# Optimization experiments

Hardware: AMD Instinct MI355X
Metric: run time of the kernel (lower is better)

The kernel has to match this reference:

```python
import jax, jax.numpy as jnp
import numpy as np

B = 131072
NF, E = 9, 8
D0 = NF * E  # 72
H = 64       # expert hidden
O = 8        # expert output
T, SE, SH = 3, 3, 3
VOCAB = 160000

PARAM_SHAPES = {
    "emb_table": (VOCAB, E),
    "spec0_W1": (T, SE, D0, H), "spec0_b1": (T, SE, H),
    "spec0_W2": (T, SE, H, O),  "spec0_b2": (T, SE, O),
    "shar0_W1": (SH, D0, H),    "shar0_b1": (SH, H),
    "shar0_W2": (SH, H, O),     "shar0_b2": (SH, O),
    "gate0_W1": (T, D0, H),     "gate0_b1": (T, H),
    "gate0_W2": (T, H, O),      "gate0_b2": (T, O),
    "gate0_W3": (T, O, SE + SH),
    "sgate0_W1": (D0, H), "sgate0_b1": (H,),
    "sgate0_W2": (H, O),  "sgate0_b2": (O,),
    "sgate0_W3": (O, T * SE + SH),
    "spec1_W1": (T, SE, O, H), "spec1_b1": (T, SE, H),
    "spec1_W2": (T, SE, H, O), "spec1_b2": (T, SE, O),
    "shar1_W1": (SH, O, H),    "shar1_b1": (SH, H),
    "shar1_W2": (SH, H, O),    "shar1_b2": (SH, O),
    "gate1_W1": (T, O, H),     "gate1_b1": (T, H),
    "gate1_W2": (T, H, O),     "gate1_b2": (T, O),
    "gate1_W3": (T, O, SE + SH),
    "tower_W": (T, O, 1), "tower_b": (T, 1),
}


def setup_inputs() -> dict:
    key = jax.random.key(0)
    keys = jax.random.split(key, len(PARAM_SHAPES) + 1)
    inp = {n: jax.random.normal(k, s, jnp.float32) * 0.1
           for (n, s), k in zip(PARAM_SHAPES.items(), keys[:-1])}
    inp["cat_idx"] = jax.random.randint(keys[-1], (B, NF), 0, VOCAB, jnp.int32)
    return inp


def _cgc(task_x, shared_x, sW1, sb1, sW2, sb2, hW1, hb1, hW2, hb2,
         gW1, gb1, gW2, gb2, gW3, sgate=None):
    """One CGC level. task_x: [T,B,in], shared_x: [B,in]."""
    # task-specific experts, batched over (task, expert)
    h = jax.nn.relu(jnp.einsum('tbi,teih->tebh', task_x, sW1) + sb1[:, :, None, :])
    spec = jax.nn.relu(jnp.einsum('tebh,teho->tebo', h, sW2) + sb2[:, :, None, :])  # [T,SE,B,O]
    # shared experts, batched over expert
    hs = jax.nn.relu(jnp.einsum('bi,eih->ebh', shared_x, hW1) + hb1[:, None, :])
    shar = jax.nn.relu(jnp.einsum('ebh,eho->ebo', hs, hW2) + hb2[:, None, :])       # [SH,B,O]
    # per-task gates: MLP[64,8] relu -> linear(no bias) -> softmax over SE+SH experts
    g = jax.nn.relu(jnp.einsum('tbi,tih->tbh', task_x, gW1) + gb1[:, None, :])
    g = jax.nn.relu(jnp.einsum('tbh,tho->tbo', g, gW2) + gb2[:, None, :])
    gw = jax.nn.softmax(jnp.einsum('tbo,toe->tbe', g, gW3), axis=-1)                # [T,B,SE+SH]
    experts = jnp.concatenate(
        [spec, jnp.broadcast_to(shar[None], (spec.shape[0],) + shar.shape)], axis=1)  # [T,SE+SH,B,O]
    task_out = jnp.einsum('tebo,tbe->tbo', experts, gw)                             # [T,B,O]
    if sgate is None:
        return task_out, None
    sgW1, sgb1, sgW2, sgb2, sgW3 = sgate
    gs = jax.nn.relu(shared_x @ sgW1 + sgb1)
    gs = jax.nn.relu(gs @ sgW2 + sgb2)
    gws = jax.nn.softmax(gs @ sgW3, axis=-1)                                        # [B,T*SE+SH]
    all_e = jnp.concatenate([spec.reshape(T * SE, spec.shape[2], O), shar], axis=0)  # [T*SE+SH,B,O]
    shared_out = jnp.einsum('ebo,be->bo', all_e, gws)
    return task_out, shared_out


def _forward(cat_idx, p):
    x = p["emb_table"][cat_idx].reshape(cat_idx.shape[0], -1)  # [B, 72]
    task_x = jnp.broadcast_to(x[None], (T,) + x.shape)
    task_x, shared_x = _cgc(
        task_x, x,
        p["spec0_W1"], p["spec0_b1"], p["spec0_W2"], p["spec0_b2"],
        p["shar0_W1"], p["shar0_b1"], p["shar0_W2"], p["shar0_b2"],
        p["gate0_W1"], p["gate0_b1"], p["gate0_W2"], p["gate0_b2"], p["gate0_W3"],
        sgate=(p["sgate0_W1"], p["sgate0_b1"], p["sgate0_W2"], p["sgate0_b2"], p["sgate0_W3"]))
    task_x, _ = _cgc(
        task_x, shared_x,
        p["spec1_W1"], p["spec1_b1"], p["spec1_W2"], p["spec1_b2"],
        p["shar1_W1"], p["shar1_b1"], p["shar1_W2"], p["shar1_b2"],
        p["gate1_W1"], p["gate1_b1"], p["gate1_W2"], p["gate1_b2"], p["gate1_W3"],
        sgate=None)
    # 3 sigmoid towers -> stacked [T, B, 1] (== dict task_0..task_2 in original)
    out = jax.nn.sigmoid(jnp.einsum('tbo,tok->tbk', task_x, p["tower_W"]) + p["tower_b"][:, None, :])
    return out


def reference(cat_idx, emb_table, spec0_W1, spec0_b1, spec0_W2, spec0_b2,
              shar0_W1, shar0_b1, shar0_W2, shar0_b2,
              gate0_W1, gate0_b1, gate0_W2, gate0_b2, gate0_W3,
              sgate0_W1, sgate0_b1, sgate0_W2, sgate0_b2, sgate0_W3,
              spec1_W1, spec1_b1, spec1_W2, spec1_b2,
              shar1_W1, shar1_b1, shar1_W2, shar1_b2,
              gate1_W1, gate1_b1, gate1_W2, gate1_b2, gate1_W3,
              tower_W, tower_b):
    p = dict(locals())
    p.pop('cat_idx')
    return _forward(cat_idx, p)
```

## Files before the change

kernel.cpp:

```cpp
#include <hip/hip_runtime.h>
#include <hip/hip_bf16.h>


#define NT 256
#define EPB 64

typedef unsigned short u16;
typedef unsigned int u32;
typedef __attribute__((ext_vector_type(8))) short short8;
typedef __attribute__((ext_vector_type(4))) float floatx4;

__device__ __forceinline__ float bflo(u32 w){ return __uint_as_float(w << 16); }
__device__ __forceinline__ float bfhi(u32 w){ return __uint_as_float(w & 0xffff0000u); }
__device__ __forceinline__ u32 f2bf(float f){
  u32 v = __float_as_uint(f);
  return (v + 0x7fffu + ((v>>16)&1u)) >> 16;
}
__device__ __forceinline__ u32 pk2(float a, float b){
  __hip_bfloat162 h2 = __float22bfloat162_rn(make_float2(a, b));
  u32 r; __builtin_memcpy(&r, &h2, sizeof(r)); return r;
}

__device__ __forceinline__ int pi_h(int s){
  return (s&1)*16 + (s>>1) + ((s>=32) ? 16 : 0);
}

#define W1F0 0
#define W2F0 49152
#define W1F1 57344
#define W2F1 72704
#define OFF_b1P0 80384
#define OFF_b2P0 81408
#define OFF_b1P1 81664
#define OFF_b2P1 82624
#define OFF_G0W3 82864
#define OFF_SG0W3 83008
#define OFF_G1W3 83104
#define OFF_TW   83248
#define OFF_Tb   83272
#define CVT_TOTAL 83275

struct PSrc { const float* p[33]; };

__global__ void cvt_kernel(PSrc S, u32* __restrict__ wsU, float* __restrict__ wsF){
  int i = blockIdx.x*256 + threadIdx.x;
  if (i >= CVT_TOTAL) return;
  if (i < 49152){
    int j2 = i & 3, l = (i>>2)&63, tt = (i>>8)&3;
    int rest = i >> 10; int s = rest % 3, u = rest / 3;
    int k0 = s*32 + (l>>4)*8 + 2*j2;
    int h  = tt*16 + (l&15);
    const float* src = (u<9)  ? S.p[0]  + (u*72)*64
                     : (u<12) ? S.p[4]  + ((u-9)*72)*64
                     : (u<15) ? S.p[8]  + ((u-12)*72)*64
                              : S.p[13];
    float lo = (k0   < 72) ? src[(k0  )*64 + h] : 0.f;
    float hi = (k0+1 < 72) ? src[(k0+1)*64 + h] : 0.f;
    wsU[i] = pk2(lo, hi);
    return;
  }
  i -= 49152;
  if (i < 8192){
    int j2 = i & 3, l = (i>>2)&63, ks = (i>>8)&1, u = i>>9;
    int s0 = ks*32 + (l>>4)*8 + 2*j2;
    int n = l & 15;
    const float* src = (u<9)  ? S.p[2]  + u*512
                     : (u<12) ? S.p[6]  + (u-9)*512
                     : (u<15) ? S.p[10] + (u-12)*512
                              : S.p[15];
    float lo = (n<8) ? src[pi_h(s0  )*8 + n] : 0.f;
    float hi = (n<8) ? src[pi_h(s0+1)*8 + n] : 0.f;
    wsU[W2F0 + i] = pk2(lo, hi);
    return;
  }
  i -= 8192;
  if (i < 15360){
    int j2 = i & 3, l = (i>>2)&63, tt = (i>>8)&3, u = i>>10;
    int k0 = (l>>4)*8 + 2*j2;
    int n = tt*16 + (l&15);
    const float* src = (u<9) ? S.p[18] + (u*8)*64
                     : (u<12) ? S.p[22] + ((u-9)*8)*64
                              : S.p[26] + ((u-12)*8)*64;
    float lo = (k0   < 8) ? src[(k0  )*64 + n] : 0.f;
    float hi = (k0+1 < 8) ? src[(k0+1)*64 + n] : 0.f;
    wsU[W1F1 + i] = pk2(lo, hi);
    return;
  }
  i -= 15360;
  if (i < 7680){
    int j2 = i & 3, l = (i>>2)&63, ks = (i>>8)&1, u = i>>9;
    int s0 = ks*32 + (l>>4)*8 + 2*j2;
    int n = l & 15;
    const float* src = (u<9) ? S.p[20] + u*512
                     : (u<12) ? S.p[24] + (u-9)*512
                              : S.p[28] + (u-12)*512;
    float lo = (n<8) ? src[pi_h(s0  )*8 + n] : 0.f;
    float hi = (n<8) ? src[pi_h(s0+1)*8 + n] : 0.f;
    wsU[W2F1 + i] = pk2(lo, hi);
    return;
  }
  i -= 7680;
  if (i < 1024){
    int u = i>>6;
    const float* src = (u<9) ? S.p[1]+u*64 : (u<12) ? S.p[5]+(u-9)*64
                     : (u<15) ? S.p[9]+(u-12)*64 : S.p[14];
    wsF[OFF_b1P0 + i] = src[i&63];
    return;
  }
  i -= 1024;
  if (i < 256){
    int u = i>>4, n = i&15;
    const float* src = (u<9) ? S.p[3]+u*8 : (u<12) ? S.p[7]+(u-9)*8
                     : (u<15) ? S.p[11]+(u-12)*8 : S.p[16];
    wsF[OFF_b2P0 + i] = (n<8) ? src[n] : 0.f;
    return;
  }
  i -= 256;
  if (i < 960){
    int u = i>>6;
    const float* src = (u<9) ? S.p[19]+u*64 : (u<12) ? S.p[23]+(u-9)*64
                               : S.p[27]+(u-12)*64;
    wsF[OFF_b1P1 + i] = src[i&63];
    return;
  }
  i -= 960;
  if (i < 240){
    int u = i>>4, n = i&15;
    const float* src = (u<9) ? S.p[21]+u*8 : (u<12) ? S.p[25]+(u-9)*8
                               : S.p[29]+(u-12)*8;
    wsF[OFF_b2P1 + i] = (n<8) ? src[n] : 0.f;
    return;
  }
  i -= 240;
  if (i < 144){ wsF[OFF_G0W3 + i] = S.p[12][i]; return; }
  i -= 144;
  if (i < 96){ wsF[OFF_SG0W3 + i] = S.p[17][i]; return; }
  i -= 96;
  if (i < 144){ wsF[OFF_G1W3 + i] = S.p[30][i]; return; }
  i -= 144;
  if (i < 24){ wsF[OFF_TW + i] = S.p[31][i]; return; }
  i -= 24;
  wsF[OFF_Tb + i] = S.p[32][i];
}

template<int N>
__device__ __forceinline__ void softmaxT(float (&v)[N]){
  float m = v[0];
  #pragma unroll
  for (int i=1;i<N;i++) m = fmaxf(m, v[i]);
  float s = 0.f;
  #pragma unroll
  for (int i=0;i<N;i++){ v[i] = __expf(v[i]-m); s += v[i]; }
  float inv = 1.f/s;
  #pragma unroll
  for (int i=0;i<N;i++) v[i] *= inv;
}

__global__ __launch_bounds__(NT, 4) void ple_kernel(
    const float* __restrict__ emb, const int* __restrict__ cat,
    const u32* __restrict__ wsU, const float* __restrict__ P,
    float* __restrict__ out, int Btot)
{
  __shared__ u32 S_[9536];
  u32* xsA = S_;
  u32* ob  = S_ + 3072;
  u32* hbW = S_ + 7232;
  const int tid = threadIdx.x;
  const int e = tid & 63;
  const int su = __builtin_amdgcn_readfirstlane(tid >> 6);
  const int lane = tid & 63;
  const int q = lane >> 4;
  const int c16 = lane & 15;

  {
    const int eg = blockIdx.x*EPB + e;
    auto ldf = [&](int f){
      int idx = cat[eg*9 + f];
      const float* ep = emb + (long)idx*8;
      float4 a = *(const float4*)ep;
      float4 b = *(const float4*)(ep+4);
      u32* row = xsA + e*48 + f*4;
      row[0] = pk2(a.x, a.y); row[1] = pk2(a.z, a.w);
      row[2] = pk2(b.x, b.y); row[3] = pk2(b.z, b.w);
    };
    ldf(su); ldf(su+4);
    if (su == 0) ldf(8);
    u32* zr = xsA + e*48 + 36 + su*3;
    zr[0] = 0; zr[1] = 0; zr[2] = 0;
  }
  __syncthreads();

  {
    u32* hbU = hbW + su*576;
    #pragma unroll 1
    for (int k4 = 0; k4 < 4; k4++){
      const int u = su*4 + k4;
      short8 bf[3][4];
      #pragma unroll
      for (int s=0;s<3;s++)
        #pragma unroll
        for (int t=0;t<4;t++)
          bf[s][t] = *(const short8*)(wsU + W1F0 + (((u*3+s)*4+t)*64 + lane)*4);
      float bias[4];
      #pragma unroll
      for (int t=0;t<4;t++) bias[t] = P[OFF_b1P0 + u*64 + t*16 + c16];
      const float ob2 = P[OFF_b2P0 + u*16 + c16];
      short8 w2f[2];
      #pragma unroll
      for (int ks=0;ks<2;ks++)
        w2f[ks] = *(const short8*)(wsU + W2F0 + ((u*2+ks)*64 + lane)*4);

      #pragma unroll 1
      for (int m=0;m<4;m++){
        short8 af[3];
        #pragma unroll
        for (int s=0;s<3;s++)
          af[s] = *(const short8*)(xsA + (m*16 + c16)*48 + s*16 + q*4);
        floatx4 acc[4];
        #pragma unroll
        for (int t=0;t<4;t++) acc[t] = (floatx4){bias[t],bias[t],bias[t],bias[t]};
        #pragma unroll
        for (int s=0;s<3;s++)
          #pragma unroll
          for (int t=0;t<4;t++)
            acc[t] = __builtin_amdgcn_mfma_f32_16x16x32_bf16(af[s], bf[s][t], acc[t], 0,0,0);
        #pragma unroll
        for (int r=0;r<4;r++){
          hbU[(q*4+r)*36 + c16]      = pk2(fmaxf(acc[0][r],0.f), fmaxf(acc[1][r],0.f));
          hbU[(q*4+r)*36 + 16 + c16] = pk2(fmaxf(acc[2][r],0.f), fmaxf(acc[3][r],0.f));
        }
        floatx4 oc = (floatx4){ob2, ob2, ob2, ob2};
        #pragma unroll
        for (int ks=0;ks<2;ks++){
          short8 haf = *(const short8*)(hbU + c16*36 + ks*16 + q*4);
          oc = __builtin_amdgcn_mfma_f32_16x16x32_bf16(haf, w2f[ks], oc, 0,0,0);
        }
        if (c16 < 8){
          u16* obp = (u16*)ob;
          #pragma unroll
          for (int r=0;r<4;r++)
            obp[(u*4 + (c16>>1))*130 + (m*16 + q*4 + r)*2 + (c16&1)] =
                (u16)f2bf(fmaxf(oc[r], 0.f));
        }
      }
    }
  }
  __syncthreads();

  u32* l1in = xsA;
  #pragma unroll
  for (int j=0;j<4;j++) l1in[e*36 + 16 + su*4 + j] = 0;
  if (su < 3){
    const int t = su;
    float g8[8];
    #pragma unroll
    for (int jw=0;jw<4;jw++){
      u32 w = ob[((12+t)*4+jw)*65 + e];
      g8[2*jw] = bflo(w); g8[2*jw+1] = bfhi(w);
    }
    float lg[6];
    #pragma unroll
    for (int m=0;m<6;m++){
      float s = 0.f;
      #pragma unroll
      for (int j=0;j<8;j++) s = fmaf(g8[j], P[OFF_G0W3 + t*48 + j*6 + m], s);
      lg[m] = s;
    }
    softmaxT<6>(lg);
    float in8[8] = {0,0,0,0,0,0,0,0};
    #pragma unroll
    for (int x=0;x<6;x++){
      const int uu = (x<3) ? t*3+x : 9+(x-3);
      float wv = lg[x];
      #pragma unroll
      for (int jw=0;jw<4;jw++){
        u32 w = ob[(uu*4+jw)*65 + e];
        in8[2*jw]   = fmaf(wv, bflo(w), in8[2*jw]);
        in8[2*jw+1] = fmaf(wv, bfhi(w), in8[2*jw+1]);
      }
    }
    #pragma unroll
    for (int jw=0;jw<4;jw++)
      l1in[e*36 + t*4 + jw] = pk2(in8[2*jw], in8[2*jw+1]);
  } else {
    float g8[8];
    #pragma unroll
    for (int jw=0;jw<4;jw++){
      u32 w = ob[(15*4+jw)*65 + e];
      g8[2*jw] = bflo(w); g8[2*jw+1] = bfhi(w);
    }
    float lw[12];
    #pragma unroll
    for (int m=0;m<12;m++){
      float s = 0.f;
      #pragma unroll
      for (int j=0;j<8;j++) s = fmaf(g8[j], P[OFF_SG0W3 + j*12 + m], s);
      lw[m] = s;
    }
    softmaxT<12>(lw);
    float in8[8] = {0,0,0,0,0,0,0,0};
    #pragma unroll
    for (int uu=0;uu<12;uu++){
      float wv = lw[uu];
      #pragma unroll
      for (int jw=0;jw<4;jw++){
        u32 w = ob[(uu*4+jw)*65 + e];
        in8[2*jw]   = fmaf(wv, bflo(w), in8[2*jw]);
        in8[2*jw+1] = fmaf(wv, bfhi(w), in8[2*jw+1]);
      }
    }
    #pragma unroll
    for (int jw=0;jw<4;jw++)
      l1in[e*36 + 12 + jw] = pk2(in8[2*jw], in8[2*jw+1]);
  }
  __syncthreads();

  {
    u32* hbU = hbW + su*576;
    #pragma unroll 1
    for (int k4=0;k4<4;k4++){
      const int u = su*4 + k4;
      if (u >= 15) break;
      const int base_u = (u<9) ? (u/3)*4 : ((u<12) ? 12 : (u-12)*4);
      const int aoff = (q==0) ? base_u : (16 + q*4);
      short8 bf1[4];
      #pragma unroll
      for (int t=0;t<4;t++)
        bf1[t] = *(const short8*)(wsU + W1F1 + ((u*4+t)*64 + lane)*4);
      float bias[4];
      #pragma unroll
      for (int t=0;t<4;t++) bias[t] = P[OFF_b1P1 + u*64 + t*16 + c16];
      const float ob2 = P[OFF_b2P1 + u*16 + c16];
      short8 w2f[2];
      #pragma unroll
      for (int ks=0;ks<2;ks++)
        w2f[ks] = *(const short8*)(wsU + W2F1 + ((u*2+ks)*64 + lane)*4);

      #pragma unroll 1
      for (int m=0;m<4;m++){
        short8 af = *(const short8*)(l1in + (m*16 + c16)*36 + aoff);
        floatx4 acc[4];
        #pragma unroll
        for (int t=0;t<4;t++) acc[t] = (floatx4){bias[t],bias[t],bias[t],bias[t]};
        #pragma unroll
        for (int t=0;t<4;t++)
          acc[t] = __builtin_amdgcn_mfma_f32_16x16x32_bf16(af, bf1[t], acc[t], 0,0,0);
        #pragma unroll
        for (int r=0;r<4;r++){
          hbU[(q*4+r)*36 + c16]      = pk2(fmaxf(acc[0][r],0.f), fmaxf(acc[1][r],0.f));
          hbU[(q*4+r)*36 + 16 + c16] = pk2(fmaxf(acc[2][r],0.f), fmaxf(acc[3][r],0.f));
        }
        floatx4 oc = (floatx4){ob2, ob2, ob2, ob2};
        #pragma unroll
        for (int ks=0;ks<2;ks++){
          short8 haf = *(const short8*)(hbU + c16*36 + ks*16 + q*4);
          oc = __builtin_amdgcn_mfma_f32_16x16x32_bf16(haf, w2f[ks], oc, 0,0,0);
        }
        if (c16 < 8){
          u16* obp = (u16*)ob;
          #pragma unroll
          for (int r=0;r<4;r++)
            obp[(u*4 + (c16>>1))*130 + (m*16 + q*4 + r)*2 + (c16&1)] =
                (u16)f2bf(fmaxf(oc[r], 0.f));
        }
      }
    }
  }
  __syncthreads();

  if (su < 3){
    const int t = su;
    float g8[8];
    #pragma unroll
    for (int jw=0;jw<4;jw++){
      u32 w = ob[((12+t)*4+jw)*65 + e];
      g8[2*jw] = bflo(w); g8[2*jw+1] = bfhi(w);
    }
    float lg[6];
    #pragma unroll
    for (int m=0;m<6;m++){
      float s = 0.f;
      #pragma unroll
      for (int j=0;j<8;j++) s = fmaf(g8[j], P[OFF_G1W3 + t*48 + j*6 + m], s);
      lg[m] = s;
    }
    softmaxT<6>(lg);
    float t1[8] = {0,0,0,0,0,0,0,0};
    #pragma unroll
    for (int x=0;x<6;x++){
      const int uu = (x<3) ? t*3+x : 9+(x-3);
      float wv = lg[x];
      #pragma unroll
      for (int jw=0;jw<4;jw++){
        u32 w = ob[(uu*4+jw)*65 + e];
        t1[2*jw]   = fmaf(wv, bflo(w), t1[2*jw]);
        t1[2*jw+1] = fmaf(wv, bfhi(w), t1[2*jw+1]);
      }
    }
    float s = P[OFF_Tb + t];
    #pragma unroll
    for (int j=0;j<8;j++) s = fmaf(t1[j], P[OFF_TW + t*8 + j], s);
    out[t*Btot + blockIdx.x*EPB + e] = 1.f/(1.f + __expf(-s));
  }
}

extern "C" void kernel_launch(void* const* d_in, const int* in_sizes, int n_in,
                              void* d_out, int out_size, void* d_ws, size_t ws_size,
                              hipStream_t stream)
{
  const float* emb = (const float*)d_in[0];
  const int* cat = (const int*)d_in[34];
  float* out = (float*)d_out;
  u32* wsU = (u32*)d_ws;
  float* wsF = (float*)d_ws;
  PSrc S;
  for (int k=0;k<33;k++) S.p[k] = (const float*)d_in[k+1];
  const int B = in_sizes[34] / 9;

  cvt_kernel<<<(CVT_TOTAL+255)/256, 256, 0, stream>>>(S, wsU, wsF);
  ple_kernel<<<B/EPB, NT, 0, stream>>>(emb, cat, wsU, wsF, out, B);
}
```

Before: 193.7 us.

## Transpose expert-output LDS buffer and vectorize shared-memory accesses

Changes the shared-memory layout of expert outputs to an element-major, padded layout so the gate/combine stage reads each expert's 8 outputs with one 128-bit LDS load. Also widens the embedding staging and hidden-activation stores to uint4/uint2, changing the row stride and the W2 permutation (pi2) to match the new packed hidden layout. The aim is fewer LDS instructions and fewer bank conflicts, at the cost of slightly more shared memory per block and a reworked index mapping that must stay consistent between the host-side weight repack and the kernel.

```diff
diff --git a/kernel.cpp b/kernel.cpp
--- a/kernel.cpp
+++ b/kernel.cpp
@@ -21,8 +21,8 @@
   u32 r; __builtin_memcpy(&r, &h2, sizeof(r)); return r;
 }
 
-__device__ __forceinline__ int pi_h(int s){
-  return (s&1)*16 + (s>>1) + ((s>=32) ? 16 : 0);
+__device__ __forceinline__ int pi2(int s){
+  return (s & 3)*16 + (s >> 2);
 }
 
 #define W1F0 0
@@ -68,8 +68,8 @@
                      : (u<12) ? S.p[6]  + (u-9)*512
                      : (u<15) ? S.p[10] + (u-12)*512
                               : S.p[15];
-    float lo = (n<8) ? src[pi_h(s0  )*8 + n] : 0.f;
-    float hi = (n<8) ? src[pi_h(s0+1)*8 + n] : 0.f;
+    float lo = (n<8) ? src[pi2((s0  )&63)*8 + n] : 0.f;
+    float hi = (n<8) ? src[pi2((s0+1)&63)*8 + n] : 0.f;
     wsU[W2F0 + i] = pk2(lo, hi);
     return;
   }
@@ -94,8 +94,8 @@
     const float* src = (u<9) ? S.p[20] + u*512
                      : (u<12) ? S.p[24] + (u-9)*512
                               : S.p[28] + (u-12)*512;
-    float lo = (n<8) ? src[pi_h(s0  )*8 + n] : 0.f;
-    float hi = (n<8) ? src[pi_h(s0+1)*8 + n] : 0.f;
+    float lo = (n<8) ? src[pi2((s0  )&63)*8 + n] : 0.f;
+    float hi = (n<8) ? src[pi2((s0+1)&63)*8 + n] : 0.f;
     wsU[W2F1 + i] = pk2(lo, hi);
     return;
   }
@@ -161,10 +161,10 @@
     const u32* __restrict__ wsU, const float* __restrict__ P,
     float* __restrict__ out, int Btot)
 {
-  __shared__ u32 S_[9536];
+  __shared__ u32 S_[9984];
   u32* xsA = S_;
-  u32* ob  = S_ + 3072;
-  u32* hbW = S_ + 7232;
+  u32* obT = S_ + 3328;
+  u32* hbW = S_ + 7680;
   const int tid = threadIdx.x;
   const int e = tid & 63;
   const int su = __builtin_amdgcn_readfirstlane(tid >> 6);
@@ -179,16 +179,17 @@
       const float* ep = emb + (long)idx*8;
       float4 a = *(const float4*)ep;
       float4 b = *(const float4*)(ep+4);
-      u32* row = xsA + e*48 + f*4;
-      row[0] = pk2(a.x, a.y); row[1] = pk2(a.z, a.w);
-      row[2] = pk2(b.x, b.y); row[3] = pk2(b.z, b.w);
+      uint4 w; w.x = pk2(a.x,a.y); w.y = pk2(a.z,a.w);
+      w.z = pk2(b.x,b.y); w.w = pk2(b.z,b.w);
+      *(uint4*)(xsA + e*52 + f*4) = w;
     };
     ldf(su); ldf(su+4);
     if (su == 0) ldf(8);
-    u32* zr = xsA + e*48 + 36 + su*3;
-    zr[0] = 0; zr[1] = 0; zr[2] = 0;
+    *(uint4*)(xsA + e*52 + 36 + su*4) = (uint4){0,0,0,0};
   }
   __syncthreads();
+
+  u16* obp = (u16*)obT;
 
   {
     u32* hbU = hbW + su*576;
@@ -215,7 +216,7 @@
         short8 af[3];
         #pragma unroll
         for (int s=0;s<3;s++)
-          af[s] = *(const short8*)(xsA + (m*16 + c16)*48 + s*16 + q*4);
+          af[s] = *(const short8*)(xsA + (m*16 + c16)*52 + s*16 + q*4);
         floatx4 acc[4];
         #pragma unroll
         for (int t=0;t<4;t++) acc[t] = (floatx4){bias[t],bias[t],bias[t],bias[t]};
@@ -226,8 +227,10 @@
             acc[t] = __builtin_amdgcn_mfma_f32_16x16x32_bf16(af[s], bf[s][t], acc[t], 0,0,0);
         #pragma unroll
         for (int r=0;r<4;r++){
-          hbU[(q*4+r)*36 + c16]      = pk2(fmaxf(acc[0][r],0.f), fmaxf(acc[1][r],0.f));
-          hbU[(q*4+r)*36 + 16 + c16] = pk2(fmaxf(acc[2][r],0.f), fmaxf(acc[3][r],0.f));
+          uint2 hw;
+          hw.x = pk2(fmaxf(acc[0][r],0.f), fmaxf(acc[1][r],0.f));
+          hw.y = pk2(fmaxf(acc[2][r],0.f), fmaxf(acc[3][r],0.f));
+          *(uint2*)(hbU + (q*4+r)*36 + 2*c16) = hw;
         }
         floatx4 oc = (floatx4){ob2, ob2, ob2, ob2};
         #pragma unroll
@@ -236,11 +239,9 @@
           oc = __builtin_amdgcn_mfma_f32_16x16x32_bf16(haf, w2f[ks], oc, 0,0,0);
         }
         if (c16 < 8){
-          u16* obp = (u16*)ob;
           #pragma unroll
           for (int r=0;r<4;r++)
-            obp[(u*4 + (c16>>1))*130 + (m*16 + q*4 + r)*2 + (c16&1)] =
-                (u16)f2bf(fmaxf(oc[r], 0.f));
+            obp[(m*16 + q*4 + r)*136 + u*8 + c16] = (u16)f2bf(fmaxf(oc[r], 0.f));
         }
       }
     }
@@ -248,16 +249,12 @@
   __syncthreads();
 
   u32* l1in = xsA;
-  #pragma unroll
-  for (int j=0;j<4;j++) l1in[e*36 + 16 + su*4 + j] = 0;
+  *(uint4*)(l1in + e*36 + 16 + su*4) = (uint4){0,0,0,0};
   if (su < 3){
     const int t = su;
-    float g8[8];
-    #pragma unroll
-    for (int jw=0;jw<4;jw++){
-      u32 w = ob[((12+t)*4+jw)*65 + e];
-      g8[2*jw] = bflo(w); g8[2*jw+1] = bfhi(w);
-    }
+    uint4 gw = *(const uint4*)(obT + e*68 + (12+t)*4);
+    float g8[8] = {bflo(gw.x),bfhi(gw.x),bflo(gw.y),bfhi(gw.y),
+                   bflo(gw.z),bfhi(gw.z),bflo(gw.w),bfhi(gw.w)};
     float lg[6];
     #pragma unroll
     for (int m=0;m<6;m++){
@@ -272,23 +269,19 @@
     for (int x=0;x<6;x++){
       const int uu = (x<3) ? t*3+x : 9+(x-3);
       float wv = lg[x];
-      #pragma unroll
-      for (int jw=0;jw<4;jw++){
-        u32 w = ob[(uu*4+jw)*65 + e];
-        in8[2*jw]   = fmaf(wv, bflo(w), in8[2*jw]);
-        in8[2*jw+1] = fmaf(wv, bfhi(w), in8[2*jw+1]);
-      }
-    }
-    #pragma unroll
-    for (int jw=0;jw<4;jw++)
-      l1in[e*36 + t*4 + jw] = pk2(in8[2*jw], in8[2*jw+1]);
+      uint4 ow = *(const uint4*)(obT + e*68 + uu*4);
+      in8[0] = fmaf(wv, bflo(ow.x), in8[0]); in8[1] = fmaf(wv, bfhi(ow.x), in8[1]);
+      in8[2] = fmaf(wv, bflo(ow.y), in8[2]); in8[3] = fmaf(wv, bfhi(ow.y), in8[3]);
+      in8[4] = fmaf(wv, bflo(ow.z), in8[4]); in8[5] = fmaf(wv, bfhi(ow.z), in8[5]);
+      in8[6] = fmaf(wv, bflo(ow.w), in8[6]); in8[7] = fmaf(wv, bfhi(ow.w), in8[7]);
+    }
+    uint4 lw4; lw4.x = pk2(in8[0],in8[1]); lw4.y = pk2(in8[2],in8[3]);
+    lw4.z = pk2(in8[4],in8[5]); lw4.w = pk2(in8[6],in8[7]);
+    *(uint4*)(l1in + e*36 + t*4) = lw4;
   } else {
-    float g8[8];
-    #pragma unroll
-    for (int jw=0;jw<4;jw++){
-      u32 w = ob[(15*4+jw)*65 + e];
-      g8[2*jw] = bflo(w); g8[2*jw+1] = bfhi(w);
-    }
+    uint4 gw = *(const uint4*)(obT + e*68 + 15*4);
+    float g8[8] = {bflo(gw.x),bfhi(gw.x),bflo(gw.y),bfhi(gw.y),
+                   bflo(gw.z),bfhi(gw.z),bflo(gw.w),bfhi(gw.w)};
     float lw[12];
     #pragma unroll
     for (int m=0;m<12;m++){
@@ -302,16 +295,15 @@
     #pragma unroll
     for (int uu=0;uu<12;uu++){
       float wv = lw[uu];
-      #pragma unroll
-      for (int jw=0;jw<4;jw++){
-        u32 w = ob[(uu*4+jw)*65 + e];
-        in8[2*jw]   = fmaf(wv, bflo(w), in8[2*jw]);
-        in8[2*jw+1] = fmaf(wv, bfhi(w), in8[2*jw+1]);
-      }
-    }
-    #pragma unroll
-    for (int jw=0;jw<4;jw++)
-      l1in[e*36 + 12 + jw] = pk2(in8[2*jw], in8[2*jw+1]);
+      uint4 ow = *(const uint4*)(obT + e*68 + uu*4);
+      in8[0] = fmaf(wv, bflo(ow.x), in8[0]); in8[1] = fmaf(wv, bfhi(ow.x), in8[1]);
+      in8[2] = fmaf(wv, bflo(ow.y), in8[2]); in8[3] = fmaf(wv, bfhi(ow.y), in8[3]);
+      in8[4] = fmaf(wv, bflo(ow.z), in8[4]); in8[5] = fmaf(wv, bfhi(ow.z), in8[5]);
+      in8[6] = fmaf(wv, bflo(ow.w), in8[6]); in8[7] = fmaf(wv, bfhi(ow.w), in8[7]);
+    }
+    uint4 lw4; lw4.x = pk2(in8[0],in8[1]); lw4.y = pk2(in8[2],in8[3]);
+    lw4.z = pk2(in8[4],in8[5]); lw4.w = pk2(in8[6],in8[7]);
+    *(uint4*)(l1in + e*36 + 12) = lw4;
   }
   __syncthreads();
 
@@ -347,8 +339,10 @@
           acc[t] = __builtin_amdgcn_mfma_f32_16x16x32_bf16(af, bf1[t], acc[t], 0,0,0);
         #pragma unroll
         for (int r=0;r<4;r++){
-          hbU[(q*4+r)*36 + c16]      = pk2(fmaxf(acc[0][r],0.f), fmaxf(acc[1][r],0.f));
-          hbU[(q*4+r)*36 + 16 + c16] = pk2(fmaxf(acc[2][r],0.f), fmaxf(acc[3][r],0.f));
+          uint2 hw;
+          hw.x = pk2(fmaxf(acc[0][r],0.f), fmaxf(acc[1][r],0.f));
+          hw.y = pk2(fmaxf(acc[2][r],0.f), fmaxf(acc[3][r],0.f));
+          *(uint2*)(hbU + (q*4+r)*36 + 2*c16) = hw;
         }
         floatx4 oc = (floatx4){ob2, ob2, ob2, ob2};
         #pragma unroll
@@ -357,11 +351,9 @@
           oc = __builtin_amdgcn_mfma_f32_16x16x32_bf16(haf, w2f[ks], oc, 0,0,0);
         }
         if (c16 < 8){
-          u16* obp = (u16*)ob;
           #pragma unroll
           for (int r=0;r<4;r++)
-            obp[(u*4 + (c16>>1))*130 + (m*16 + q*4 + r)*2 + (c16&1)] =
-                (u16)f2bf(fmaxf(oc[r], 0.f));
+            obp[(m*16 + q*4 + r)*136 + u*8 + c16] = (u16)f2bf(fmaxf(oc[r], 0.f));
         }
       }
     }
@@ -370,12 +362,9 @@
 
   if (su < 3){
     const int t = su;
-    float g8[8];
-    #pragma unroll
-    for (int jw=0;jw<4;jw++){
-      u32 w = ob[((12+t)*4+jw)*65 + e];
-      g8[2*jw] = bflo(w); g8[2*jw+1] = bfhi(w);
-    }
+    uint4 gw = *(const uint4*)(obT + e*68 + (12+t)*4);
+    float g8[8] = {bflo(gw.x),bfhi(gw.x),bflo(gw.y),bfhi(gw.y),
+                   bflo(gw.z),bfhi(gw.z),bflo(gw.w),bfhi(gw.w)};
     float lg[6];
     #pragma unroll
     for (int m=0;m<6;m++){
@@ -390,12 +379,11 @@
     for (int x=0;x<6;x++){
       const int uu = (x<3) ? t*3+x : 9+(x-3);
       float wv = lg[x];
-      #pragma unroll
-      for (int jw=0;jw<4;jw++){
-        u32 w = ob[(uu*4+jw)*65 + e];
-        t1[2*jw]   = fmaf(wv, bflo(w), t1[2*jw]);
-        t1[2*jw+1] = fmaf(wv, bfhi(w), t1[2*jw+1]);
-      }
+      uint4 ow = *(const uint4*)(obT + e*68 + uu*4);
+      t1[0] = fmaf(wv, bflo(ow.x), t1[0]); t1[1] = fmaf(wv, bfhi(ow.x), t1[1]);
+      t1[2] = fmaf(wv, bflo(ow.y), t1[2]); t1[3] = fmaf(wv, bfhi(ow.y), t1[3]);
+      t1[4] = fmaf(wv, bflo(ow.z), t1[4]); t1[5] = fmaf(wv, bfhi(ow.z), t1[5]);
+      t1[6] = fmaf(wv, bflo(ow.w), t1[6]); t1[7] = fmaf(wv, bfhi(ow.w), t1[7]);
     }
     float s = P[OFF_Tb + t];
     #pragma unroll
```

New measurement: 194.9 us. Within noise of the previous version (+0.6%).
